# Kernel optimization log

Hardware: AMD Instinct MI355X
Metric: run time of the kernel (lower is better)

Reference implementation:

```python
import jax, jax.numpy as jnp
import numpy as np

NODE_DIM = 256
EDGE_DIM = 32
HIDDEN = 128
N_NODES = 100000
N_EDGES = 1000000


def setup_inputs() -> dict:
    key = jax.random.key(0)
    k_z, k_ei, k_ea, k_w1, k_b1, k_w2, k_b2 = jax.random.split(key, 7)
    in_dim = NODE_DIM * 2 + EDGE_DIM
    z = jax.random.normal(k_z, (N_NODES, NODE_DIM), dtype=jnp.float32)
    edge_label_index = jax.random.randint(k_ei, (2, N_EDGES), 0, N_NODES, dtype=jnp.int64)
    edge_attr = jax.random.normal(k_ea, (N_EDGES, EDGE_DIM), dtype=jnp.float32)
    # nn.Linear-style init: U(-1/sqrt(fan_in), 1/sqrt(fan_in))
    s1 = 1.0 / np.sqrt(in_dim)
    s2 = 1.0 / np.sqrt(HIDDEN)
    W1 = jax.random.uniform(k_w1, (in_dim, HIDDEN), jnp.float32, -s1, s1)
    b1 = jax.random.uniform(k_b1, (HIDDEN,), jnp.float32, -s1, s1)
    W2 = jax.random.uniform(k_w2, (HIDDEN, 1), jnp.float32, -s2, s2)
    b2 = jax.random.uniform(k_b2, (1,), jnp.float32, -s2, s2)
    return {"z": z, "edge_label_index": edge_label_index, "edge_attr": edge_attr,
            "W1": W1, "b1": b1, "W2": W2, "b2": b2}


def reference(z, edge_label_index, edge_attr, W1, b1, W2, b2):
    src = edge_label_index[0]
    dst = edge_label_index[1]
    # [E, 2*node_dim + edge_dim] concatenated edge features
    feat = jnp.concatenate([z[src], z[dst], edge_attr], axis=-1)
    h = jax.nn.relu(feat @ W1 + b1)          # [E, 128]
    out = h @ W2 + b2                        # [E, 1]
    return out.reshape(-1)                   # [E]
```

## Files before the change

kernel.cpp:

```cpp
#include <hip/hip_runtime.h>

typedef __attribute__((ext_vector_type(8))) short short8;
typedef __attribute__((ext_vector_type(8))) unsigned short ushort8;
typedef __attribute__((ext_vector_type(4))) float f32x4;

__device__ __forceinline__ unsigned short f2bf(float f) {
  unsigned int u = __float_as_uint(f);
  u += 0x7fffu + ((u >> 16) & 1u);
  return (unsigned short)(u >> 16);
}
__device__ __forceinline__ float bf2f(unsigned short u) {
  return __uint_as_float(((unsigned int)u) << 16);
}
__device__ __forceinline__ void gl_lds16(const void* g, void* l) {
  __builtin_amdgcn_global_load_lds(
      (const __attribute__((address_space(1))) unsigned int*)g,
      (__attribute__((address_space(3))) unsigned int*)l, 16, 0, 0);
}

__global__ void prep_weights(const float* __restrict__ W1,
                             unsigned short* __restrict__ W1T2,
                             unsigned short* __restrict__ W1cT) {
  int idx = blockIdx.x * 256 + threadIdx.x;
  if (idx < 65536) {
    int np = idx >> 8, k = idx & 255;
    W1T2[idx] = f2bf(W1[(size_t)(k + ((np >> 7) << 8)) * 128 + (np & 127)]);
  } else if (idx < 65536 + 4096) {
    int j = idx - 65536;
    int n = j >> 5, k = j & 31;
    W1cT[j] = f2bf(W1[(size_t)(512 + k) * 128 + n]);
  }
}

__global__ __launch_bounds__(256, 2) void node_proj(
    const float* __restrict__ z, const unsigned short* __restrict__ W1T2,
    unsigned short* __restrict__ Ps, int NN) {
  __shared__ unsigned short As[2][128 * 32];
  __shared__ unsigned short Bs[2][256 * 32];
  const int tid = threadIdx.x, wid = tid >> 6, lane = tid & 63;
  const int wrow = wid >> 1, wcol = wid & 1;
  const int quad = lane >> 4, l15 = lane & 15;
  const int lrow = lane >> 2, lch = lane & 3;
  const int bm = blockIdx.x;

  const float* zsrc[2];
  int rr[2];
#pragma unroll
  for (int j = 0; j < 2; ++j) {
    rr[j] = (2 * wid + j) * 16 + lrow;
    int node = min(bm * 128 + rr[j], NN - 1);
    zsrc[j] = z + (size_t)node * 256;
  }

  f32x4 acc[4][8] = {};

  auto stage = [&](int ks, int bb) {
#pragma unroll
    for (int j = 0; j < 4; ++j) {
      int nb = 4 * wid + j;
      gl_lds16(W1T2 + (size_t)(nb * 16 + lrow) * 256 + ks * 32 + lch * 8,
               &Bs[bb][nb * 512]);
    }
#pragma unroll
    for (int j = 0; j < 2; ++j) {
      const float* g = zsrc[j] + ks * 32 + lch * 8;
      f32x4 a = *(const f32x4*)g;
      f32x4 c = *(const f32x4*)(g + 4);
      ushort8 o;
      o[0]=f2bf(a[0]); o[1]=f2bf(a[1]); o[2]=f2bf(a[2]); o[3]=f2bf(a[3]);
      o[4]=f2bf(c[0]); o[5]=f2bf(c[1]); o[6]=f2bf(c[2]); o[7]=f2bf(c[3]);
      *(ushort8*)&As[bb][rr[j] * 32 + lch * 8] = o;
    }
  };

  auto compute = [&](int bb) {
    short8 af[4], bfv[8];
#pragma unroll
    for (int i = 0; i < 4; ++i)
      af[i] = *(const short8*)&As[bb][(wrow * 64 + i * 16 + l15) * 32 + quad * 8];
#pragma unroll
    for (int i = 0; i < 8; ++i)
      bfv[i] = *(const short8*)&Bs[bb][(wcol * 128 + i * 16 + l15) * 32 + quad * 8];
#pragma unroll
    for (int mi = 0; mi < 4; ++mi)
#pragma unroll
      for (int ni = 0; ni < 8; ++ni)
        acc[mi][ni] = __builtin_amdgcn_mfma_f32_16x16x32_bf16(af[mi], bfv[ni], acc[mi][ni], 0, 0, 0);
  };

  stage(0, 0);
#pragma unroll 1
  for (int s = 0; s < 8; ++s) {
    __syncthreads();
    if (s + 1 < 8) stage(s + 1, (s + 1) & 1);
    compute(s & 1);
  }

#pragma unroll
  for (int mi = 0; mi < 4; ++mi) {
#pragma unroll
    for (int r = 0; r < 4; ++r) {
      int row = wrow * 64 + mi * 16 + quad * 4 + r;
      int node = bm * 128 + row;
      if (node < NN) {
        ushort8 o;
#pragma unroll
        for (int ni = 0; ni < 8; ++ni) o[ni] = f2bf(acc[mi][ni][r]);
        *(ushort8*)&Ps[(size_t)node * 256 + wcol * 128 + l15 * 8] = o;
      }
    }
  }
}

__global__ __launch_bounds__(256, 3) void edge_pred(
    const int* __restrict__ eidx, const float* __restrict__ ea,
    const unsigned short* __restrict__ Ps, const unsigned short* __restrict__ W1cT,
    const float* __restrict__ b1, const float* __restrict__ W2,
    const float* __restrict__ b2, float* __restrict__ out, int E) {
  const int tid = threadIdx.x, wid = tid >> 6, lane = tid & 63;
  const int quad = lane >> 4, l15 = lane & 15;
  const int ebase = blockIdx.x * 128 + wid * 32;

  int srcn[8], dstn[8];
#pragma unroll
  for (int t = 0; t < 8; ++t) {
    int ec = min(ebase + (t >> 2) * 16 + quad * 4 + (t & 3), E - 1);
    srcn[t] = eidx[ec];
    dstn[t] = eidx[E + ec];
  }

  f32x4 ealo[2], eahi[2];
#pragma unroll
  for (int mi = 0; mi < 2; ++mi) {
    const float* g = ea + (size_t)min(ebase + mi * 16 + l15, E - 1) * 32 + quad * 8;
    ealo[mi] = __builtin_nontemporal_load((const f32x4*)g);
    eahi[mi] = __builtin_nontemporal_load((const f32x4*)(g + 4));
  }

  short8 bfv[8];
#pragma unroll
  for (int ni = 0; ni < 8; ++ni)
    bfv[ni] = *(const short8*)&W1cT[(ni * 16 + l15) * 32 + quad * 8];

  float b1v[8], w2v[8];
#pragma unroll
  for (int ni = 0; ni < 8; ++ni) {
    int c = ni * 16 + l15;
    b1v[ni] = b1[c];
    w2v[ni] = W2[c];
  }
  const float b2v = b2[0];

  short8 p1[8], p2[8];
#pragma unroll
  for (int t = 0; t < 8; ++t) {
    p1[t] = *(const short8*)&Ps[(size_t)srcn[t] * 256 + l15 * 8];
    p2[t] = *(const short8*)&Ps[(size_t)dstn[t] * 256 + 128 + l15 * 8];
  }

  short8 af[2];
#pragma unroll
  for (int mi = 0; mi < 2; ++mi) {
    ushort8 o;
    o[0]=f2bf(ealo[mi][0]); o[1]=f2bf(ealo[mi][1]); o[2]=f2bf(ealo[mi][2]); o[3]=f2bf(ealo[mi][3]);
    o[4]=f2bf(eahi[mi][0]); o[5]=f2bf(eahi[mi][1]); o[6]=f2bf(eahi[mi][2]); o[7]=f2bf(eahi[mi][3]);
    af[mi] = (short8)o;
  }

  f32x4 acc[2][8] = {};
#pragma unroll
  for (int mi = 0; mi < 2; ++mi)
#pragma unroll
    for (int ni = 0; ni < 8; ++ni)
      acc[mi][ni] = __builtin_amdgcn_mfma_f32_16x16x32_bf16(af[mi], bfv[ni], acc[mi][ni], 0, 0, 0);

#pragma unroll
  for (int mi = 0; mi < 2; ++mi) {
#pragma unroll
    for (int r = 0; r < 4; ++r) {
      int t = mi * 4 + r;
      float p = 0.f;
#pragma unroll
      for (int ni = 0; ni < 8; ++ni) {
        float s = bf2f((unsigned short)p1[t][ni]) + bf2f((unsigned short)p2[t][ni]);
        float h = acc[mi][ni][r] + s + b1v[ni];
        h = fmaxf(h, 0.f);
        p = fmaf(h, w2v[ni], p);
      }
      p += __shfl_xor(p, 1);
      p += __shfl_xor(p, 2);
      p += __shfl_xor(p, 4);
      p += __shfl_xor(p, 8);
      int e = ebase + mi * 16 + quad * 4 + r;
      if (l15 == 0 && e < E) out[e] = p + b2v;
    }
  }
}

extern "C" void kernel_launch(void* const* d_in, const int* in_sizes, int n_in,
                              void* d_out, int out_size, void* d_ws, size_t ws_size,
                              hipStream_t stream) {
  const float* z   = (const float*)d_in[0];
  const int*   eix = (const int*)d_in[1];
  const float* ea  = (const float*)d_in[2];
  const float* W1  = (const float*)d_in[3];
  const float* b1  = (const float*)d_in[4];
  const float* W2  = (const float*)d_in[5];
  const float* b2  = (const float*)d_in[6];
  float* out = (float*)d_out;

  const int E  = in_sizes[1] / 2;
  const int NN = in_sizes[0] / 256;

  unsigned short* wsp = (unsigned short*)d_ws;
  unsigned short* Ps   = wsp;
  unsigned short* W1T2 = wsp + (size_t)NN * 256;
  unsigned short* W1cT = W1T2 + 65536;

  prep_weights<<<273, 256, 0, stream>>>(W1, W1T2, W1cT);

  int nbm = (NN + 127) / 128;
  node_proj<<<nbm, 256, 0, stream>>>(z, W1T2, Ps, NN);

  int ge = (E + 127) / 128;
  edge_pred<<<ge, 256, 0, stream>>>(eix, ea, Ps, W1cT, b1, W2, b2, out, E);
}
```

Measured before the change: 337.6 us.

## Use fragment-major LDS layout and halve per-wave edge tiles for occupancy

node_proj now stages A and B tiles in LDS in MFMA-fragment order, so each lane reads a contiguous 16-byte chunk at lane*8. This is meant to cut LDS bank conflicts during the fragment loads. edge_pred now handles 16 edges per wave instead of 32, with launch bounds raised to 4 blocks per SM, to lower register pressure and hide gather latency with more waves. b1 and W2 are pre-swizzled in prep_weights so each lane loads its 8 values as two vector loads, and outputs use nontemporal stores. The tradeoff is that the W1cT fragment and the bias/weight loads are repeated across twice as many blocks.

```diff
diff --git a/kernel.cpp b/kernel.cpp
--- a/kernel.cpp
+++ b/kernel.cpp
@@ -19,16 +19,26 @@
 }
 
 __global__ void prep_weights(const float* __restrict__ W1,
+                             const float* __restrict__ b1,
+                             const float* __restrict__ W2,
                              unsigned short* __restrict__ W1T2,
-                             unsigned short* __restrict__ W1cT) {
+                             unsigned short* __restrict__ W1cT,
+                             float* __restrict__ b1s,
+                             float* __restrict__ W2s) {
   int idx = blockIdx.x * 256 + threadIdx.x;
   if (idx < 65536) {
     int np = idx >> 8, k = idx & 255;
     W1T2[idx] = f2bf(W1[(size_t)(k + ((np >> 7) << 8)) * 128 + (np & 127)]);
-  } else if (idx < 65536 + 4096) {
+  } else if (idx < 69632) {
     int j = idx - 65536;
     int n = j >> 5, k = j & 31;
     W1cT[j] = f2bf(W1[(size_t)(512 + k) * 128 + n]);
+  } else if (idx < 69760) {
+    int j = idx - 69632;
+    b1s[j] = b1[(j & 7) * 16 + (j >> 3)];
+  } else if (idx < 69888) {
+    int j = idx - 69760;
+    W2s[j] = W2[(j & 7) * 16 + (j >> 3)];
   }
 }
 
@@ -40,15 +50,13 @@
   const int tid = threadIdx.x, wid = tid >> 6, lane = tid & 63;
   const int wrow = wid >> 1, wcol = wid & 1;
   const int quad = lane >> 4, l15 = lane & 15;
-  const int lrow = lane >> 2, lch = lane & 3;
   const int bm = blockIdx.x;
 
   const float* zsrc[2];
-  int rr[2];
 #pragma unroll
   for (int j = 0; j < 2; ++j) {
-    rr[j] = (2 * wid + j) * 16 + lrow;
-    int node = min(bm * 128 + rr[j], NN - 1);
+    int row = (2 * wid + j) * 16 + l15;
+    int node = min(bm * 128 + row, NN - 1);
     zsrc[j] = z + (size_t)node * 256;
   }
 
@@ -58,18 +66,18 @@
 #pragma unroll
     for (int j = 0; j < 4; ++j) {
       int nb = 4 * wid + j;
-      gl_lds16(W1T2 + (size_t)(nb * 16 + lrow) * 256 + ks * 32 + lch * 8,
+      gl_lds16(W1T2 + (size_t)(nb * 16 + l15) * 256 + ks * 32 + quad * 8,
                &Bs[bb][nb * 512]);
     }
 #pragma unroll
     for (int j = 0; j < 2; ++j) {
-      const float* g = zsrc[j] + ks * 32 + lch * 8;
-      f32x4 a = *(const f32x4*)g;
-      f32x4 c = *(const f32x4*)(g + 4);
+      const float* gp = zsrc[j] + ks * 32 + quad * 8;
+      f32x4 a = *(const f32x4*)gp;
+      f32x4 c = *(const f32x4*)(gp + 4);
       ushort8 o;
       o[0]=f2bf(a[0]); o[1]=f2bf(a[1]); o[2]=f2bf(a[2]); o[3]=f2bf(a[3]);
       o[4]=f2bf(c[0]); o[5]=f2bf(c[1]); o[6]=f2bf(c[2]); o[7]=f2bf(c[3]);
-      *(ushort8*)&As[bb][rr[j] * 32 + lch * 8] = o;
+      *(ushort8*)&As[bb][(2 * wid + j) * 512 + lane * 8] = o;
     }
   };
 
@@ -77,10 +85,10 @@
     short8 af[4], bfv[8];
 #pragma unroll
     for (int i = 0; i < 4; ++i)
-      af[i] = *(const short8*)&As[bb][(wrow * 64 + i * 16 + l15) * 32 + quad * 8];
+      af[i] = *(const short8*)&As[bb][(wrow * 4 + i) * 512 + lane * 8];
 #pragma unroll
     for (int i = 0; i < 8; ++i)
-      bfv[i] = *(const short8*)&Bs[bb][(wcol * 128 + i * 16 + l15) * 32 + quad * 8];
+      bfv[i] = *(const short8*)&Bs[bb][(wcol * 8 + i) * 512 + lane * 8];
 #pragma unroll
     for (int mi = 0; mi < 4; ++mi)
 #pragma unroll
@@ -112,88 +120,73 @@
   }
 }
 
-__global__ __launch_bounds__(256, 3) void edge_pred(
+__global__ __launch_bounds__(256, 4) void edge_pred(
     const int* __restrict__ eidx, const float* __restrict__ ea,
     const unsigned short* __restrict__ Ps, const unsigned short* __restrict__ W1cT,
-    const float* __restrict__ b1, const float* __restrict__ W2,
+    const float* __restrict__ b1s, const float* __restrict__ W2s,
     const float* __restrict__ b2, float* __restrict__ out, int E) {
   const int tid = threadIdx.x, wid = tid >> 6, lane = tid & 63;
   const int quad = lane >> 4, l15 = lane & 15;
-  const int ebase = blockIdx.x * 128 + wid * 32;
-
-  int srcn[8], dstn[8];
-#pragma unroll
-  for (int t = 0; t < 8; ++t) {
-    int ec = min(ebase + (t >> 2) * 16 + quad * 4 + (t & 3), E - 1);
+  const int ebase = blockIdx.x * 64 + wid * 16;
+
+  int srcn[4], dstn[4];
+#pragma unroll
+  for (int t = 0; t < 4; ++t) {
+    int ec = min(ebase + quad * 4 + t, E - 1);
     srcn[t] = eidx[ec];
     dstn[t] = eidx[E + ec];
   }
 
-  f32x4 ealo[2], eahi[2];
-#pragma unroll
-  for (int mi = 0; mi < 2; ++mi) {
-    const float* g = ea + (size_t)min(ebase + mi * 16 + l15, E - 1) * 32 + quad * 8;
-    ealo[mi] = __builtin_nontemporal_load((const f32x4*)g);
-    eahi[mi] = __builtin_nontemporal_load((const f32x4*)(g + 4));
-  }
+  const float* g = ea + (size_t)min(ebase + l15, E - 1) * 32 + quad * 8;
+  f32x4 ealo = __builtin_nontemporal_load((const f32x4*)g);
+  f32x4 eahi = __builtin_nontemporal_load((const f32x4*)(g + 4));
 
   short8 bfv[8];
 #pragma unroll
   for (int ni = 0; ni < 8; ++ni)
     bfv[ni] = *(const short8*)&W1cT[(ni * 16 + l15) * 32 + quad * 8];
 
-  float b1v[8], w2v[8];
-#pragma unroll
-  for (int ni = 0; ni < 8; ++ni) {
-    int c = ni * 16 + l15;
-    b1v[ni] = b1[c];
-    w2v[ni] = W2[c];
-  }
-  const float b2v = b2[0];
-
-  short8 p1[8], p2[8];
-#pragma unroll
-  for (int t = 0; t < 8; ++t) {
+  short8 p1[4], p2[4];
+#pragma unroll
+  for (int t = 0; t < 4; ++t) {
     p1[t] = *(const short8*)&Ps[(size_t)srcn[t] * 256 + l15 * 8];
     p2[t] = *(const short8*)&Ps[(size_t)dstn[t] * 256 + 128 + l15 * 8];
   }
 
-  short8 af[2];
-#pragma unroll
-  for (int mi = 0; mi < 2; ++mi) {
-    ushort8 o;
-    o[0]=f2bf(ealo[mi][0]); o[1]=f2bf(ealo[mi][1]); o[2]=f2bf(ealo[mi][2]); o[3]=f2bf(ealo[mi][3]);
-    o[4]=f2bf(eahi[mi][0]); o[5]=f2bf(eahi[mi][1]); o[6]=f2bf(eahi[mi][2]); o[7]=f2bf(eahi[mi][3]);
-    af[mi] = (short8)o;
-  }
-
-  f32x4 acc[2][8] = {};
-#pragma unroll
-  for (int mi = 0; mi < 2; ++mi)
-#pragma unroll
-    for (int ni = 0; ni < 8; ++ni)
-      acc[mi][ni] = __builtin_amdgcn_mfma_f32_16x16x32_bf16(af[mi], bfv[ni], acc[mi][ni], 0, 0, 0);
-
-#pragma unroll
-  for (int mi = 0; mi < 2; ++mi) {
-#pragma unroll
-    for (int r = 0; r < 4; ++r) {
-      int t = mi * 4 + r;
-      float p = 0.f;
-#pragma unroll
-      for (int ni = 0; ni < 8; ++ni) {
-        float s = bf2f((unsigned short)p1[t][ni]) + bf2f((unsigned short)p2[t][ni]);
-        float h = acc[mi][ni][r] + s + b1v[ni];
-        h = fmaxf(h, 0.f);
-        p = fmaf(h, w2v[ni], p);
-      }
-      p += __shfl_xor(p, 1);
-      p += __shfl_xor(p, 2);
-      p += __shfl_xor(p, 4);
-      p += __shfl_xor(p, 8);
-      int e = ebase + mi * 16 + quad * 4 + r;
-      if (l15 == 0 && e < E) out[e] = p + b2v;
-    }
+  ushort8 o;
+  o[0]=f2bf(ealo[0]); o[1]=f2bf(ealo[1]); o[2]=f2bf(ealo[2]); o[3]=f2bf(ealo[3]);
+  o[4]=f2bf(eahi[0]); o[5]=f2bf(eahi[1]); o[6]=f2bf(eahi[2]); o[7]=f2bf(eahi[3]);
+  short8 af = (short8)o;
+
+  f32x4 acc[8] = {};
+#pragma unroll
+  for (int ni = 0; ni < 8; ++ni)
+    acc[ni] = __builtin_amdgcn_mfma_f32_16x16x32_bf16(af, bfv[ni], acc[ni], 0, 0, 0);
+
+  f32x4 b1a = *(const f32x4*)&b1s[l15 * 8];
+  f32x4 b1b = *(const f32x4*)&b1s[l15 * 8 + 4];
+  f32x4 w2a = *(const f32x4*)&W2s[l15 * 8];
+  f32x4 w2b = *(const f32x4*)&W2s[l15 * 8 + 4];
+  const float b2v = b2[0];
+
+#pragma unroll
+  for (int r = 0; r < 4; ++r) {
+    float p = 0.f;
+#pragma unroll
+    for (int ni = 0; ni < 8; ++ni) {
+      float s = bf2f((unsigned short)p1[r][ni]) + bf2f((unsigned short)p2[r][ni]);
+      float bb = (ni < 4) ? b1a[ni] : b1b[ni - 4];
+      float ww = (ni < 4) ? w2a[ni] : w2b[ni - 4];
+      float h = acc[ni][r] + s + bb;
+      h = fmaxf(h, 0.f);
+      p = fmaf(h, ww, p);
+    }
+    p += __shfl_xor(p, 1);
+    p += __shfl_xor(p, 2);
+    p += __shfl_xor(p, 4);
+    p += __shfl_xor(p, 8);
+    int e = ebase + quad * 4 + r;
+    if (l15 == 0 && e < E) __builtin_nontemporal_store(p + b2v, &out[e]);
   }
 }
 
@@ -216,12 +209,14 @@
   unsigned short* Ps   = wsp;
   unsigned short* W1T2 = wsp + (size_t)NN * 256;
   unsigned short* W1cT = W1T2 + 65536;
-
-  prep_weights<<<273, 256, 0, stream>>>(W1, W1T2, W1cT);
+  float* b1s = (float*)(W1cT + 4096);
+  float* W2s = b1s + 128;
+
+  prep_weights<<<273, 256, 0, stream>>>(W1, b1, W2, W1T2, W1cT, b1s, W2s);
 
   int nbm = (NN + 127) / 128;
   node_proj<<<nbm, 256, 0, stream>>>(z, W1T2, Ps, NN);
 
-  int ge = (E + 127) / 128;
-  edge_pred<<<ge, 256, 0, stream>>>(eix, ea, Ps, W1cT, b1, W2, b2, out, E);
-}
+  int ge = (E + 63) / 64;
+  edge_pred<<<ge, 256, 0, stream>>>(eix, ea, Ps, W1cT, b1s, W2s, b2, out, E);
+}
```

After: 339.0 us. Within noise of the previous version (+0.4%).
